# Kernel optimization log

Measured on AMD Instinct MI355X. Metric: run time of the kernel, lower is better.

The kernel has to match this reference:

```python
import jax, jax.numpy as jnp
import numpy as np

C1, C2, NUM_HEADS = 128, 128, 8
N, H_A, W_A = 2, 200, 200
H_B, W_B = 100, 360


def _polar_coords(fov, gh, gw, H, W):
    # Pixel-space polar sampling grid, matching torch linspace semantics.
    cx, cy = W // 2, H // 2
    t = jnp.arange(gw, dtype=jnp.float32) / (gw - 1)
    angles = -fov / 2 + fov * t                      # [gw]
    ca, sa = jnp.cos(angles), jnp.sin(angles)
    rmax = jnp.minimum(cx / jnp.abs(ca), cy / jnp.abs(sa))
    r = (jnp.arange(gh, dtype=jnp.float32) / (gh - 1))[:, None] * rmax[None, :]  # [gh,gw]
    x = jnp.clip(cx + r * ca, 0.0, W - 1.0)
    y = jnp.clip(cy - r * sa, 0.0, H - 1.0)
    return x, y


def _bilinear(bev, x, y):
    # grid_sample(mode='bilinear', align_corners=True) with in-range clamped coords.
    C, H, W = bev.shape
    x0 = jnp.floor(x); y0 = jnp.floor(y)
    wx = x - x0; wy = y - y0
    x0i = jnp.clip(x0.astype(jnp.int32), 0, W - 1)
    x1i = jnp.clip(x0i + 1, 0, W - 1)
    y0i = jnp.clip(y0.astype(jnp.int32), 0, H - 1)
    y1i = jnp.clip(y0i + 1, 0, H - 1)
    v00 = bev[:, y0i, x0i]; v01 = bev[:, y0i, x1i]
    v10 = bev[:, y1i, x0i]; v11 = bev[:, y1i, x1i]
    return v00 * (1 - wx) * (1 - wy) + v01 * wx * (1 - wy) + v10 * (1 - wx) * wy + v11 * wx * wy


def _restore(rect, fov, H, W):
    # scatter-add restore with count normalization (rrestore_bev_map).
    C, gh, gw = rect.shape
    x, y = _polar_coords(fov, gh, gw, H, W)
    xi = jnp.clip(jnp.round(x).astype(jnp.int32), 0, W - 1)
    yi = jnp.clip(jnp.round(y).astype(jnp.int32), 0, H - 1)
    idx = (yi * W + xi).reshape(-1)
    vals = rect.reshape(C, -1)
    acc = jnp.zeros((C, H * W), rect.dtype).at[:, idx].add(vals)
    cnt = jnp.zeros((H * W,), rect.dtype).at[idx].add(jnp.ones_like(idx, rect.dtype))
    cnt = jnp.where(cnt == 0, jnp.ones_like(cnt), cnt)
    return (acc / cnt).reshape(C, H, W)


def _mha(q, k, v, in_w, in_b, out_w, out_b, nheads):
    # torch.nn.MultiheadAttention (batch_first, eval mode -> dropout inactive).
    B, Lq, E = q.shape
    Lk = k.shape[1]
    hd = E // nheads
    wq, wk, wv = jnp.split(in_w, 3)
    bq, bk, bv = jnp.split(in_b, 3)
    qh = (q @ wq.T + bq).reshape(B, Lq, nheads, hd).transpose(0, 2, 1, 3)
    kh = (k @ wk.T + bk).reshape(B, Lk, nheads, hd).transpose(0, 2, 1, 3)
    vh = (v @ wv.T + bv).reshape(B, Lk, nheads, hd).transpose(0, 2, 1, 3)
    scores = jnp.einsum('bhqd,bhkd->bhqk', qh, kh) / jnp.sqrt(jnp.asarray(hd, q.dtype))
    attn = jax.nn.softmax(scores, axis=-1)
    o = jnp.einsum('bhqk,bhkd->bhqd', attn, vh).transpose(0, 2, 1, 3).reshape(B, Lq, E)
    return o @ out_w.T + out_b


def setup_inputs() -> dict:
    key = jax.random.key(0)
    ks = jax.random.split(key, 12)
    s1 = 1.0 / np.sqrt(C1)
    s2 = 1.0 / np.sqrt(C2)
    return {
        'list_a': jax.random.normal(ks[0], (N, C1, H_A, W_A), jnp.float32),
        'list_b': jax.random.normal(ks[1], (N, C2, H_B, W_B), jnp.float32),
        'fov_list': jax.random.uniform(ks[2], (N,), jnp.float32, 0.5 * np.pi, 0.9 * np.pi),
        'rots_list': jax.random.normal(ks[3], (N, 3, 3), jnp.float32),
        'trans_list': jax.random.normal(ks[4], (N, 3), jnp.float32),
        'Wq': jax.random.normal(ks[5], (C1, C1), jnp.float32) * s1,
        'bq': jnp.zeros((C1,), jnp.float32),
        'Wk': jax.random.normal(ks[6], (C1, C2), jnp.float32) * s2,
        'bk': jnp.zeros((C1,), jnp.float32),
        'Wv': jax.random.normal(ks[7], (C1, C2), jnp.float32) * s2,
        'bv': jnp.zeros((C1,), jnp.float32),
        'in_proj_w': jax.random.normal(ks[8], (3 * C1, C1), jnp.float32) * s1,
        'in_proj_b': jnp.zeros((3 * C1,), jnp.float32),
        'out_w': jax.random.normal(ks[9], (C1, C1), jnp.float32) * s1,
        'out_b': jnp.zeros((C1,), jnp.float32),
    }


def reference(list_a, list_b, fov_list, rots_list, trans_list,
              Wq, bq, Wk, bk, Wv, bv, in_proj_w, in_proj_b, out_w, out_b):
    def per_sample(a, b, fov):
        c1, h1, w1 = a.shape
        c2, h2, w2 = b.shape
        # extract rectangular (polar resample) of a onto (h1, w2) grid
        x, y = _polar_coords(fov, h1, w2, h1, w1)
        a_rect = _bilinear(a, x, y)                 # [C1, h1, w2]
        a_seq = a_rect.transpose(2, 1, 0)           # [w2, h1, C1]
        b_seq = b.transpose(2, 1, 0)                # [w2, h2, C2]
        q = a_seq @ Wq.T + bq
        k = b_seq @ Wk.T + bk
        v = b_seq @ Wv.T + bv
        o = _mha(q, k, v, in_proj_w, in_proj_b, out_w, out_b, NUM_HEADS)
        a_enh = o.transpose(2, 1, 0)                # [C1, h1, w2]
        return a + _restore(a_enh, fov, h1, w1)
    return jax.vmap(per_sample)(list_a, list_b, fov_list)
```

## Files before the change

kernel.cpp:

```cpp
#include <hip/hip_runtime.h>
#include <hip/hip_bf16.h>
#include <math.h>

#define C1N 128
#define HA 200
#define WA 200
#define HBB 100
#define WBB 360
#define GH 200
#define GW 360
#define NHD 8
#define HDD 16

typedef __attribute__((ext_vector_type(8))) short short8;
typedef __attribute__((ext_vector_type(4))) float f32x4;
typedef __attribute__((ext_vector_type(16))) float f32x16;

__device__ __forceinline__ float bf2f(unsigned short u) {
  union { unsigned int i; float f; } c; c.i = ((unsigned int)u) << 16; return c.f;
}
__device__ __forceinline__ unsigned short f2bf(float f) {
  __hip_bfloat16 h = __float2bfloat16(f);
  unsigned short u;
  __builtin_memcpy(&u, &h, sizeof(u));
  return u;
}

__device__ __forceinline__ void polar_xy(float fov, int i, int j, float& x, float& y) {
#pragma clang fp contract(off)
  float t = (float)j / 359.0f;
  float angle = -fov / 2.0f + fov * t;
  float ca = (float)cos((double)angle);
  float sa = (float)sin((double)angle);
  float rmax = fminf(100.0f / fabsf(ca), 100.0f / fabsf(sa));
  float r = ((float)i / 199.0f) * rmax;
  float xv = 100.0f + r * ca;
  float yv = 100.0f - r * sa;
  x = fminf(fmaxf(xv, 0.0f), 199.0f);
  y = fminf(fmaxf(yv, 0.0f), 199.0f);
}

__global__ void weff_k(const float* __restrict__ Wq, const float* __restrict__ Wk,
                       const float* __restrict__ Wv, const float* __restrict__ bq,
                       const float* __restrict__ bk, const float* __restrict__ bv,
                       const float* __restrict__ inw, const float* __restrict__ inb,
                       const float* __restrict__ outw, const float* __restrict__ outb,
                       __hip_bfloat16* __restrict__ Wb, float* __restrict__ beff) {
  int which = blockIdx.y;
  int o = blockIdx.x;
  int kcol = threadIdx.x;
  if (which == 3) {
    Wb[3 * 16384 + o * 128 + kcol] = __float2bfloat16(outw[o * 128 + kcol]);
    if (kcol == 0) beff[384 + o] = outb[o];
    return;
  }
  const float* Wx = (which == 0) ? Wq : ((which == 1) ? Wk : Wv);
  const float* bx = (which == 0) ? bq : ((which == 1) ? bk : bv);
  const float* wrow = inw + (which * 128 + o) * 128;
  float acc = 0.0f;
  for (int m = 0; m < 128; ++m) acc += wrow[m] * Wx[m * 128 + kcol];
  Wb[which * 16384 + o * 128 + kcol] = __float2bfloat16(acc);
  if (kcol == 0) {
    float bacc = inb[which * 128 + o];
    for (int m = 0; m < 128; ++m) bacc += wrow[m] * bx[m];
    beff[which * 128 + o] = bacc;
  }
}

__global__ __launch_bounds__(256) void transA_k(const float* __restrict__ a,
                                                __hip_bfloat16* __restrict__ aT) {
  __shared__ float tile[32][33];
  int p0 = blockIdx.x * 32, c0 = blockIdx.y * 32;
  int tp = threadIdx.x & 31, tr = threadIdx.x >> 5;
  for (int cc = tr; cc < 32; cc += 8)
    tile[cc][tp] = a[(size_t)(c0 + cc) * 40000 + p0 + tp];
  __syncthreads();
  for (int pp = tr; pp < 32; pp += 8)
    aT[(size_t)(p0 + pp) * C1N + c0 + tp] = __float2bfloat16(tile[tp][pp]);
}

__global__ __launch_bounds__(256) void bilinear2_k(const __hip_bfloat16* __restrict__ aT,
                                                   const float* __restrict__ fovp, int n,
                                                   __hip_bfloat16* __restrict__ aseq) {
  __shared__ float sw[20][4];
  __shared__ int sp[20][4];
  int j = blockIdx.x;
  int i_base = blockIdx.y * 20;
  int t = threadIdx.x;
  if (t < 20) {
    float x, y;
    polar_xy(fovp[n], i_base + t, j, x, y);
    float x0f = floorf(x), y0f = floorf(y);
    float wx = x - x0f, wy = y - y0f;
    int x0 = max(0, min(199, (int)x0f));
    int x1 = min(x0 + 1, 199);
    int y0 = max(0, min(199, (int)y0f));
    int y1 = min(y0 + 1, 199);
    sp[t][0] = y0 * 200 + x0; sp[t][1] = y0 * 200 + x1;
    sp[t][2] = y1 * 200 + x0; sp[t][3] = y1 * 200 + x1;
    sw[t][0] = (1.0f - wx) * (1.0f - wy); sw[t][1] = wx * (1.0f - wy);
    sw[t][2] = (1.0f - wx) * wy;          sw[t][3] = wx * wy;
  }
  __syncthreads();
  int lane = t & 63, wv = t >> 6;
  for (int ii = wv; ii < 20; ii += 4) {
    int i = i_base + ii;
    float w00 = sw[ii][0], w01 = sw[ii][1], w10 = sw[ii][2], w11 = sw[ii][3];
    ushort2 u00 = ((const ushort2*)(aT + (size_t)sp[ii][0] * C1N))[lane];
    ushort2 u01 = ((const ushort2*)(aT + (size_t)sp[ii][1] * C1N))[lane];
    ushort2 u10 = ((const ushort2*)(aT + (size_t)sp[ii][2] * C1N))[lane];
    ushort2 u11 = ((const ushort2*)(aT + (size_t)sp[ii][3] * C1N))[lane];
    float v0 = w00 * bf2f(u00.x) + w01 * bf2f(u01.x) + w10 * bf2f(u10.x) + w11 * bf2f(u11.x);
    float v1 = w00 * bf2f(u00.y) + w01 * bf2f(u01.y) + w10 * bf2f(u10.y) + w11 * bf2f(u11.y);
    ushort2 outv; outv.x = f2bf(v0); outv.y = f2bf(v1);
    ((ushort2*)(aseq + (size_t)(j * GH + i) * C1N))[lane] = outv;
  }
}

__global__ __launch_bounds__(256) void transpose_k(const float* __restrict__ b,
                                                   __hip_bfloat16* __restrict__ bs) {
  __shared__ float tile[32][33];
  int kk = blockIdx.z;
  int j0 = blockIdx.x * 32, c0 = blockIdx.y * 32;
  int tj = threadIdx.x & 31;
  int tr = threadIdx.x >> 5;
  for (int cc = tr; cc < 32; cc += 8) {
    int gj = j0 + tj;
    tile[cc][tj] = (gj < WBB) ? b[(c0 + cc) * (HBB * WBB) + kk * WBB + gj] : 0.0f;
  }
  __syncthreads();
  for (int jj = tr; jj < 32; jj += 8) {
    int gj = j0 + jj;
    if (gj < WBB)
      bs[(size_t)(gj * HBB + kk) * C1N + c0 + (threadIdx.x & 31)] =
          __float2bfloat16(tile[threadIdx.x & 31][jj]);
  }
}

__device__ __forceinline__ void gemm16_mfma(const unsigned short* __restrict__ A,
                                            const unsigned short* __restrict__ W,
                                            int m_base, f32x4 acc[8]) {
  int lane = threadIdx.x & 63;
  int col = lane & 15, quad = lane >> 4;
#pragma unroll
  for (int nt = 0; nt < 8; ++nt) acc[nt] = (f32x4)0.0f;
#pragma unroll
  for (int s = 0; s < 4; ++s) {
    short8 aF = *(const short8*)&A[(size_t)(m_base + col) * 128 + s * 32 + quad * 8];
#pragma unroll
    for (int nt = 0; nt < 8; ++nt) {
      short8 bF = *(const short8*)&W[(size_t)(nt * 16 + col) * 128 + s * 32 + quad * 8];
      acc[nt] = __builtin_amdgcn_mfma_f32_16x16x32_bf16(aF, bF, acc[nt], 0, 0, 0);
    }
  }
}

__device__ __forceinline__ void stage_bf16(unsigned short (*tile)[136],
                                           const f32x4 acc[8],
                                           const float* __restrict__ bias) {
  int lane = threadIdx.x & 63, wv = threadIdx.x >> 6;
  int col = lane & 15, quad = lane >> 4;
#pragma unroll
  for (int nt = 0; nt < 8; ++nt) {
    float bb = bias[nt * 16 + col];
#pragma unroll
    for (int r = 0; r < 4; ++r)
      tile[wv * 16 + quad * 4 + r][nt * 16 + col] = f2bf(acc[nt][r] + bb);
  }
  __syncthreads();
}

__global__ __launch_bounds__(256) void gemm_q_k(const unsigned short* __restrict__ A,
                                                const unsigned short* __restrict__ Wb,
                                                const float* __restrict__ beff,
                                                unsigned short* __restrict__ qb) {
  __shared__ unsigned short tile[64][136];
  int m0 = blockIdx.x * 64;
  f32x4 acc[8];
  gemm16_mfma(A, Wb, m0 + (threadIdx.x >> 6) * 16, acc);
  stage_bf16(tile, acc, beff);
  for (int u = threadIdx.x; u < 1024; u += 256) {
    int rl = u >> 4, ch = (u & 15) * 8;
    *(short8*)&qb[(size_t)(m0 + rl) * 128 + ch] = *(const short8*)&tile[rl][ch];
  }
}

__global__ __launch_bounds__(256) void gemm_kv_k(const unsigned short* __restrict__ A,
                                                 const unsigned short* __restrict__ Wb,
                                                 const float* __restrict__ beff,
                                                 unsigned short* __restrict__ kb,
                                                 unsigned short* __restrict__ vT) {
  __shared__ unsigned short tile[64][136];
  int which = blockIdx.y;
  int m0 = blockIdx.x * 64;
  f32x4 acc[8];
  gemm16_mfma(A, Wb + (which ? 32768 : 16384), m0 + (threadIdx.x >> 6) * 16, acc);
  stage_bf16(tile, acc, beff + (which ? 256 : 128));
  if (which == 0) {
    for (int u = threadIdx.x; u < 1024; u += 256) {
      int rl = u >> 4, ch = (u & 15) * 8;
      int row = m0 + rl;
      if (row < 36000) {
        int jj = row / 100, key = row - jj * 100;
        *(short8*)&kb[((size_t)jj * 128 + key) * 128 + ch] = *(const short8*)&tile[rl][ch];
      }
    }
  } else {
    for (int u = threadIdx.x; u < 8192; u += 256) {
      int cc = u >> 6, kl = u & 63;
      int row = m0 + kl;
      if (row < 36000) {
        int jj = row / 100, key = row - jj * 100;
        vT[((size_t)jj * 128 + cc) * 128 + key] = tile[kl][cc];
      }
    }
  }
}

__global__ __launch_bounds__(512) void attn6_k(const unsigned short* __restrict__ qb,
                                               const unsigned short* __restrict__ kb,
                                               const unsigned short* __restrict__ vT,
                                               unsigned short* __restrict__ o) {
  __shared__ unsigned short Ps[8][32][120];
  __shared__ unsigned short Osh[32][136];
  int d = blockIdx.x;
  int xcd = d & 7, idx = d >> 3;
  int j = xcd * 45 + idx % 45;
  int mt = idx / 45;
  int h = threadIdx.x >> 6;
  int lane = threadIdx.x & 63;
  int col = lane & 31, half = lane >> 5;

  short8 qF = *(const short8*)&qb[(size_t)(j * 200 + mt * 32 + col) * 128 + h * 16 + half * 8];
  f32x16 S[4];
#pragma unroll
  for (int nt = 0; nt < 4; ++nt) {
    short8 kF = *(const short8*)&kb[((size_t)j * 128 + nt * 32 + col) * 128 + h * 16 + half * 8];
    S[nt] = __builtin_amdgcn_mfma_f32_32x32x16_bf16(kF, qF, (f32x16)0.0f, 0, 0, 0);
  }

  float rsum = 0.0f;
#pragma unroll
  for (int nt = 0; nt < 3; ++nt)
#pragma unroll
    for (int r = 0; r < 16; ++r) {
      float e = __expf(S[nt][r] * 0.25f);
      S[nt][r] = e; rsum += e;
    }
#pragma unroll
  for (int r = 0; r < 16; ++r) {
    float e = (half == 0 && r < 4) ? __expf(S[3][r] * 0.25f) : 0.0f;
    S[3][r] = e; rsum += e;
  }
  rsum += __shfl_xor(rsum, 32, 64);
  float inv = __fdividef(1.0f, rsum);

#pragma unroll
  for (int nt = 0; nt < 4; ++nt) {
#pragma unroll
    for (int g = 0; g < 4; ++g) {
      if (nt == 3 && g >= 2) continue;
      float e0 = S[nt][4 * g + 0] * inv, e1 = S[nt][4 * g + 1] * inv;
      float e2 = S[nt][4 * g + 2] * inv, e3 = S[nt][4 * g + 3] * inv;
      unsigned int lo, hi;
      asm("v_cvt_pk_bf16_f32 %0, %1, %2" : "=v"(lo) : "v"(e0), "v"(e1));
      asm("v_cvt_pk_bf16_f32 %0, %1, %2" : "=v"(hi) : "v"(e2), "v"(e3));
      *(uint2*)&Ps[h][col][nt * 32 + 8 * g + 4 * half] = make_uint2(lo, hi);
    }
  }

  short8 ones;
#pragma unroll
  for (int i = 0; i < 8; ++i) ones[i] = (short)0x3F80;
  const unsigned short* vrow = &vT[((size_t)j * 128 + h * 16 + (col & 15)) * 128];
  f32x16 O = (f32x16)0.0f;
#pragma unroll
  for (int ks = 0; ks < 7; ++ks) {
    short8 aP = *(const short8*)&Ps[h][col][ks * 16 + half * 8];
    short8 bV = (col < 16) ? *(const short8*)&vrow[ks * 16 + half * 8] : ones;
    O = __builtin_amdgcn_mfma_f32_32x32x16_bf16(aP, bV, O, 0, 0, 0);
  }
#pragma unroll
  for (int r = 0; r < 16; ++r) {
    int row = (r & 3) + 8 * (r >> 2) + 4 * half;
    if (col < 16) Osh[row][h * 16 + col] = f2bf(O[r]);
  }
  __syncthreads();
  int rl = threadIdx.x >> 4, ch = (threadIdx.x & 15) * 8;
  int qr = mt * 32 + rl;
  if (qr < 200)
    *(short8*)&o[(size_t)(j * 200 + qr) * 128 + ch] = *(const short8*)&Osh[rl][ch];
}

__global__ __launch_bounds__(256) void gemm_os_k(const unsigned short* __restrict__ A,
                                                 const unsigned short* __restrict__ Wb,
                                                 const float* __restrict__ beff,
                                                 const float* __restrict__ fovp, int n,
                                                 float* __restrict__ accP,
                                                 float* __restrict__ cnt) {
  __shared__ float tile[64][132];
  __shared__ int sidx[64];
  int m0 = blockIdx.x * 64;
  int t = threadIdx.x;
  f32x4 acc[8];
  gemm16_mfma(A, Wb + 49152, m0 + (t >> 6) * 16, acc);
  if (t < 64) {
    int m = m0 + t;
    int j = m / 200, i = m - j * 200;
    float x, y;
    polar_xy(fovp[n], i, j, x, y);
    int xi = (int)rintf(x); xi = max(0, min(199, xi));
    int yi = (int)rintf(y); yi = max(0, min(199, yi));
    sidx[t] = yi * 200 + xi;
    atomicAdd(&cnt[yi * 200 + xi], 1.0f);
  }
  {
    int lane = t & 63, wv = t >> 6;
    int col = lane & 15, quad = lane >> 4;
#pragma unroll
    for (int nt = 0; nt < 8; ++nt) {
      float bb = beff[384 + nt * 16 + col];
#pragma unroll
      for (int r = 0; r < 4; ++r)
        tile[wv * 16 + quad * 4 + r][nt * 16 + col] = acc[nt][r] + bb;
    }
  }
  __syncthreads();
  int c = t & 127, half = t >> 7;
  int r0 = half * 32;
  int cur = sidx[r0];
  float sum = 0.0f;
#pragma unroll 4
  for (int r = r0; r < r0 + 32; ++r) {
    float v = tile[r][c];
    int idx = sidx[r];
    if (idx != cur) {
      atomicAdd(&accP[(size_t)cur * C1N + c], sum);
      cur = idx;
      sum = v;
    } else {
      sum += v;
    }
  }
  atomicAdd(&accP[(size_t)cur * C1N + c], sum);
}

__global__ __launch_bounds__(256) void finalize2_k(const float* __restrict__ a,
                                                   const float* __restrict__ accP,
                                                   const float* __restrict__ cnt,
                                                   float* __restrict__ out) {
  __shared__ float tile[64][129];
  __shared__ float sinv[64];
  int p0 = blockIdx.x * 64;
  int t = threadIdx.x;
  if (t < 64) {
    float cv = cnt[p0 + t];
    sinv[t] = 1.0f / (cv == 0.0f ? 1.0f : cv);
  }
  for (int u = t; u < 64 * 128; u += 256) {
    int pp = u >> 7, c = u & 127;
    tile[pp][c] = accP[(size_t)(p0 + pp) * C1N + c];
  }
  __syncthreads();
  for (int u = t; u < 64 * 128; u += 256) {
    int pp = u & 63, c = u >> 6;
    int g = c * 40000 + p0 + pp;
    out[g] = a[g] + tile[pp][c] * sinv[pp];
  }
}

extern "C" void kernel_launch(void* const* d_in, const int* in_sizes, int n_in,
                              void* d_out, int out_size, void* d_ws, size_t ws_size,
                              hipStream_t stream) {
  const float* list_a = (const float*)d_in[0];
  const float* list_b = (const float*)d_in[1];
  const float* fov   = (const float*)d_in[2];
  const float* Wq    = (const float*)d_in[5];
  const float* bq    = (const float*)d_in[6];
  const float* Wk    = (const float*)d_in[7];
  const float* bk    = (const float*)d_in[8];
  const float* Wv    = (const float*)d_in[9];
  const float* bv    = (const float*)d_in[10];
  const float* inw   = (const float*)d_in[11];
  const float* inb   = (const float*)d_in[12];
  const float* outw  = (const float*)d_in[13];
  const float* outb  = (const float*)d_in[14];
  float* out = (float*)d_out;
  float* ws = (float*)d_ws;

  float* beff = ws;
  __hip_bfloat16* Wb = (__hip_bfloat16*)(ws + 512);
  float* P2 = ws + 512 + 32768;
  float* qb_f = P2 + 9216000;
  float* kb_f = qb_f + 4620288;
  float* vT_f = kb_f + 2949120;
  float* P0_f = vT_f + 2949120;
  float* P1_f = P0_f + 4620288;
  float* cnt  = P1_f + 2310144;

  unsigned short* qb = (unsigned short*)qb_f;
  unsigned short* kb = (unsigned short*)kb_f;
  unsigned short* vT = (unsigned short*)vT_f;
  __hip_bfloat16* P0 = (__hip_bfloat16*)P0_f;
  __hip_bfloat16* P1 = (__hip_bfloat16*)P1_f;
  __hip_bfloat16* aT = (__hip_bfloat16*)P2;
  float* accP = P2;

  weff_k<<<dim3(128, 4), 128, 0, stream>>>(Wq, Wk, Wv, bq, bk, bv, inw, inb, outw, outb, Wb, beff);

  for (int n = 0; n < 2; ++n) {
    const float* a_n = list_a + (size_t)n * C1N * HA * WA;
    const float* b_n = list_b + (size_t)n * C1N * HBB * WBB;
    float* out_n = out + (size_t)n * C1N * HA * WA;

    (void)hipMemsetAsync(cnt, 0, (size_t)HA * WA * sizeof(float), stream);

    transA_k<<<dim3(1250, 4), 256, 0, stream>>>(a_n, aT);
    bilinear2_k<<<dim3(GW, 10), 256, 0, stream>>>(aT, fov, n, P0);
    (void)hipMemsetAsync(accP, 0, (size_t)HA * WA * C1N * sizeof(float), stream);
    transpose_k<<<dim3(12, 4, 100), 256, 0, stream>>>(b_n, P1);
    gemm_kv_k<<<dim3(563, 2), 256, 0, stream>>>((const unsigned short*)P1,
                                                (const unsigned short*)Wb, beff, kb, vT);
    gemm_q_k<<<1125, 256, 0, stream>>>((const unsigned short*)P0,
                                       (const unsigned short*)Wb, beff, qb);
    attn6_k<<<2520, 512, 0, stream>>>(qb, kb, vT, (unsigned short*)P0);
    gemm_os_k<<<1125, 256, 0, stream>>>((const unsigned short*)P0,
                                        (const unsigned short*)Wb, beff, fov, n,
                                        accP, cnt);
    finalize2_k<<<625, 256, 0, stream>>>(a_n, accP, cnt, out_n);
  }
}
```

Before: 507.5 us.

## Replace atomic scatter-add restore with counting-sort gather

```diff
diff --git a/kernel.cpp b/kernel.cpp
--- a/kernel.cpp
+++ b/kernel.cpp
@@ -217,6 +217,32 @@
   }
 }
 
+__global__ __launch_bounds__(256) void gemm_o_k(const unsigned short* __restrict__ A,
+                                                const unsigned short* __restrict__ Wb,
+                                                const float* __restrict__ beff,
+                                                float* __restrict__ C) {
+  __shared__ float tile[64][132];
+  int m0 = blockIdx.x * 64;
+  f32x4 acc[8];
+  gemm16_mfma(A, Wb + 49152, m0 + (threadIdx.x >> 6) * 16, acc);
+  {
+    int lane = threadIdx.x & 63, wv = threadIdx.x >> 6;
+    int col = lane & 15, quad = lane >> 4;
+#pragma unroll
+    for (int nt = 0; nt < 8; ++nt) {
+      float bb = beff[384 + nt * 16 + col];
+#pragma unroll
+      for (int r = 0; r < 4; ++r)
+        tile[wv * 16 + quad * 4 + r][nt * 16 + col] = acc[nt][r] + bb;
+    }
+  }
+  __syncthreads();
+  for (int u = threadIdx.x; u < 2048; u += 256) {
+    int rl = u >> 5, ch = (u & 31) * 4;
+    *(f32x4*)&C[(size_t)(m0 + rl) * 128 + ch] = *(const f32x4*)&tile[rl][ch];
+  }
+}
+
 __global__ __launch_bounds__(512) void attn6_k(const unsigned short* __restrict__ qb,
                                                const unsigned short* __restrict__ kb,
                                                const unsigned short* __restrict__ vT,
@@ -292,71 +318,100 @@
     *(short8*)&o[(size_t)(j * 200 + qr) * 128 + ch] = *(const short8*)&Osh[rl][ch];
 }
 
-__global__ __launch_bounds__(256) void gemm_os_k(const unsigned short* __restrict__ A,
-                                                 const unsigned short* __restrict__ Wb,
-                                                 const float* __restrict__ beff,
-                                                 const float* __restrict__ fovp, int n,
-                                                 float* __restrict__ accP,
-                                                 float* __restrict__ cnt) {
-  __shared__ float tile[64][132];
-  __shared__ int sidx[64];
-  int m0 = blockIdx.x * 64;
-  int t = threadIdx.x;
-  f32x4 acc[8];
-  gemm16_mfma(A, Wb + 49152, m0 + (t >> 6) * 16, acc);
-  if (t < 64) {
-    int m = m0 + t;
-    int j = m / 200, i = m - j * 200;
-    float x, y;
-    polar_xy(fovp[n], i, j, x, y);
-    int xi = (int)rintf(x); xi = max(0, min(199, xi));
-    int yi = (int)rintf(y); yi = max(0, min(199, yi));
-    sidx[t] = yi * 200 + xi;
-    atomicAdd(&cnt[yi * 200 + xi], 1.0f);
-  }
-  {
-    int lane = t & 63, wv = t >> 6;
-    int col = lane & 15, quad = lane >> 4;
-#pragma unroll
-    for (int nt = 0; nt < 8; ++nt) {
-      float bb = beff[384 + nt * 16 + col];
-#pragma unroll
-      for (int r = 0; r < 4; ++r)
-        tile[wv * 16 + quad * 4 + r][nt * 16 + col] = acc[nt][r] + bb;
-    }
-  }
-  __syncthreads();
-  int c = t & 127, half = t >> 7;
-  int r0 = half * 32;
-  int cur = sidx[r0];
-  float sum = 0.0f;
-#pragma unroll 4
-  for (int r = r0; r < r0 + 32; ++r) {
-    float v = tile[r][c];
-    int idx = sidx[r];
-    if (idx != cur) {
-      atomicAdd(&accP[(size_t)cur * C1N + c], sum);
-      cur = idx;
-      sum = v;
-    } else {
-      sum += v;
-    }
-  }
-  atomicAdd(&accP[(size_t)cur * C1N + c], sum);
-}
-
-__global__ __launch_bounds__(256) void finalize2_k(const float* __restrict__ a,
+__global__ __launch_bounds__(256) void count_k(const float* __restrict__ fovp, int n,
+                                               int* __restrict__ pid,
+                                               int* __restrict__ counts) {
+  int m = blockIdx.x * 256 + threadIdx.x;
+  if (m >= 72000) return;
+  int j = m / 200, i = m - j * 200;
+  float x, y;
+  polar_xy(fovp[n], i, j, x, y);
+  int xi = (int)rintf(x); xi = max(0, min(199, xi));
+  int yi = (int)rintf(y); yi = max(0, min(199, yi));
+  int p = yi * 200 + xi;
+  pid[m] = p;
+  atomicAdd(counts + p, 1);
+}
+
+__global__ __launch_bounds__(256) void sumv_k(const int* __restrict__ counts,
+                                              int* __restrict__ bsum) {
+  __shared__ int sred[4];
+  int b = blockIdx.x, t = threadIdx.x;
+  int s = 0;
+  for (int u = t; u < 1000; u += 256) s += counts[b * 1000 + u];
+  for (int off = 32; off; off >>= 1) s += __shfl_down(s, off, 64);
+  if ((t & 63) == 0) sred[t >> 6] = s;
+  __syncthreads();
+  if (t == 0) bsum[b] = sred[0] + sred[1] + sred[2] + sred[3];
+}
+
+__global__ __launch_bounds__(64) void scanf_k(const int* __restrict__ counts,
+                                              const int* __restrict__ bsum,
+                                              int* __restrict__ offs,
+                                              int* __restrict__ cursor) {
+  __shared__ int sc[1000];
+  int b = blockIdx.x, t = threadIdx.x;
+  for (int u = t; u < 1000; u += 64) sc[u] = counts[b * 1000 + u];
+  __syncthreads();
+  if (t == 0) {
+    int run = 0;
+    for (int q = 0; q < b; ++q) run += bsum[q];
+    for (int u = 0; u < 1000; ++u) { int v = sc[u]; sc[u] = run; run += v; }
+  }
+  __syncthreads();
+  for (int u = t; u < 1000; u += 64) {
+    int o = sc[u];
+    offs[b * 1000 + u] = o;
+    cursor[b * 1000 + u] = o;
+  }
+}
+
+__global__ __launch_bounds__(256) void fill_k(const int* __restrict__ pid,
+                                              int* __restrict__ cursor,
+                                              int* __restrict__ srcm) {
+  int m = blockIdx.x * 256 + threadIdx.x;
+  if (m >= 72000) return;
+  int slot = atomicAdd(cursor + pid[m], 1);
+  srcm[slot] = m;
+}
+
+__global__ __launch_bounds__(256) void gather_k(const float* __restrict__ aenh,
+                                                const int* __restrict__ offs,
+                                                const int* __restrict__ counts,
+                                                const int* __restrict__ srcm,
+                                                float* __restrict__ accP) {
+  int W = blockIdx.x * 4 + (threadIdx.x >> 6);
+  int lane = threadIdx.x & 63;
+  for (int k = 0; k < 16; ++k) {
+    int p = W + 2500 * k;
+    int nsz = counts[p], s0 = offs[p];
+    float sx = 0.0f, sy = 0.0f;
+    for (int q0 = 0; q0 < nsz; q0 += 16) {
+      const float* rp[16];
+#pragma unroll
+      for (int u = 0; u < 16; ++u) {
+        int q = min(q0 + u, nsz - 1);
+        int m = srcm[s0 + q];
+        rp[u] = aenh + (size_t)m * 128 + 2 * lane;
+      }
+#pragma unroll
+      for (int u = 0; u < 16; ++u) {
+        float2 r = *(const float2*)rp[u];
+        if (q0 + u < nsz) { sx += r.x; sy += r.y; }
+      }
+    }
+    float inv = (nsz > 0) ? 1.0f / (float)nsz : 0.0f;
+    float2 o2; o2.x = sx * inv; o2.y = sy * inv;
+    *(float2*)&accP[(size_t)p * C1N + 2 * lane] = o2;
+  }
+}
+
+__global__ __launch_bounds__(256) void finalize3_k(const float* __restrict__ a,
                                                    const float* __restrict__ accP,
-                                                   const float* __restrict__ cnt,
                                                    float* __restrict__ out) {
   __shared__ float tile[64][129];
-  __shared__ float sinv[64];
   int p0 = blockIdx.x * 64;
   int t = threadIdx.x;
-  if (t < 64) {
-    float cv = cnt[p0 + t];
-    sinv[t] = 1.0f / (cv == 0.0f ? 1.0f : cv);
-  }
   for (int u = t; u < 64 * 128; u += 256) {
     int pp = u >> 7, c = u & 127;
     tile[pp][c] = accP[(size_t)(p0 + pp) * C1N + c];
@@ -365,7 +420,7 @@
   for (int u = t; u < 64 * 128; u += 256) {
     int pp = u & 63, c = u >> 6;
     int g = c * 40000 + p0 + pp;
-    out[g] = a[g] + tile[pp][c] * sinv[pp];
+    out[g] = a[g] + tile[pp][c];
   }
 }
 
@@ -396,7 +451,6 @@
   float* vT_f = kb_f + 2949120;
   float* P0_f = vT_f + 2949120;
   float* P1_f = P0_f + 4620288;
-  float* cnt  = P1_f + 2310144;
 
   unsigned short* qb = (unsigned short*)qb_f;
   unsigned short* kb = (unsigned short*)kb_f;
@@ -404,7 +458,15 @@
   __hip_bfloat16* P0 = (__hip_bfloat16*)P0_f;
   __hip_bfloat16* P1 = (__hip_bfloat16*)P1_f;
   __hip_bfloat16* aT = (__hip_bfloat16*)P2;
-  float* accP = P2;
+  float* aenh = P2;
+  float* accP = qb_f;
+
+  int* pid    = (int*)P1_f;
+  int* counts = pid + 72000;
+  int* offs   = counts + 40000;
+  int* cursor = offs + 40000;
+  int* srcm   = cursor + 40000;
+  int* bsum   = srcm + 72000;
 
   weff_k<<<dim3(128, 4), 128, 0, stream>>>(Wq, Wk, Wv, bq, bk, bv, inw, inb, outw, outb, Wb, beff);
 
@@ -413,20 +475,23 @@
     const float* b_n = list_b + (size_t)n * C1N * HBB * WBB;
     float* out_n = out + (size_t)n * C1N * HA * WA;
 
-    (void)hipMemsetAsync(cnt, 0, (size_t)HA * WA * sizeof(float), stream);
-
     transA_k<<<dim3(1250, 4), 256, 0, stream>>>(a_n, aT);
     bilinear2_k<<<dim3(GW, 10), 256, 0, stream>>>(aT, fov, n, P0);
-    (void)hipMemsetAsync(accP, 0, (size_t)HA * WA * C1N * sizeof(float), stream);
     transpose_k<<<dim3(12, 4, 100), 256, 0, stream>>>(b_n, P1);
     gemm_kv_k<<<dim3(563, 2), 256, 0, stream>>>((const unsigned short*)P1,
                                                 (const unsigned short*)Wb, beff, kb, vT);
+    (void)hipMemsetAsync(counts, 0, 40000 * sizeof(int), stream);
+    count_k<<<282, 256, 0, stream>>>(fov, n, pid, counts);
+    sumv_k<<<40, 256, 0, stream>>>(counts, bsum);
+    scanf_k<<<40, 64, 0, stream>>>(counts, bsum, offs, cursor);
+    fill_k<<<282, 256, 0, stream>>>(pid, cursor, srcm);
+
     gemm_q_k<<<1125, 256, 0, stream>>>((const unsigned short*)P0,
                                        (const unsigned short*)Wb, beff, qb);
     attn6_k<<<2520, 512, 0, stream>>>(qb, kb, vT, (unsigned short*)P0);
-    gemm_os_k<<<1125, 256, 0, stream>>>((const unsigned short*)P0,
-                                        (const unsigned short*)Wb, beff, fov, n,
-                                        accP, cnt);
-    finalize2_k<<<625, 256, 0, stream>>>(a_n, accP, cnt, out_n);
-  }
-}
+    gemm_o_k<<<1125, 256, 0, stream>>>((const unsigned short*)P0,
+                                       (const unsigned short*)Wb, beff, aenh);
+    gather_k<<<625, 256, 0, stream>>>(aenh, offs, counts, srcm, accP);
+    finalize3_k<<<625, 256, 0, stream>>>(a_n, accP, out_n);
+  }
+}
```

After: 728.1 us. 43.5% more time.

## Fuse Q projection GEMM into attention kernel and write output in place

Applied to the files above, without the earlier changes.

```diff
diff --git a/kernel.cpp b/kernel.cpp
--- a/kernel.cpp
+++ b/kernel.cpp
@@ -170,21 +170,6 @@
   __syncthreads();
 }
 
-__global__ __launch_bounds__(256) void gemm_q_k(const unsigned short* __restrict__ A,
-                                                const unsigned short* __restrict__ Wb,
-                                                const float* __restrict__ beff,
-                                                unsigned short* __restrict__ qb) {
-  __shared__ unsigned short tile[64][136];
-  int m0 = blockIdx.x * 64;
-  f32x4 acc[8];
-  gemm16_mfma(A, Wb, m0 + (threadIdx.x >> 6) * 16, acc);
-  stage_bf16(tile, acc, beff);
-  for (int u = threadIdx.x; u < 1024; u += 256) {
-    int rl = u >> 4, ch = (u & 15) * 8;
-    *(short8*)&qb[(size_t)(m0 + rl) * 128 + ch] = *(const short8*)&tile[rl][ch];
-  }
-}
-
 __global__ __launch_bounds__(256) void gemm_kv_k(const unsigned short* __restrict__ A,
                                                  const unsigned short* __restrict__ Wb,
                                                  const float* __restrict__ beff,
@@ -217,12 +202,13 @@
   }
 }
 
-__global__ __launch_bounds__(512) void attn6_k(const unsigned short* __restrict__ qb,
+__global__ __launch_bounds__(512) void attn7_k(unsigned short* __restrict__ aseq_o,
                                                const unsigned short* __restrict__ kb,
                                                const unsigned short* __restrict__ vT,
-                                               unsigned short* __restrict__ o) {
+                                               const unsigned short* __restrict__ Wb,
+                                               const float* __restrict__ beff) {
   __shared__ unsigned short Ps[8][32][120];
-  __shared__ unsigned short Osh[32][136];
+  __shared__ unsigned short qos[32][136];
   int d = blockIdx.x;
   int xcd = d & 7, idx = d >> 3;
   int j = xcd * 45 + idx % 45;
@@ -230,8 +216,36 @@
   int h = threadIdx.x >> 6;
   int lane = threadIdx.x & 63;
   int col = lane & 31, half = lane >> 5;
-
-  short8 qF = *(const short8*)&qb[(size_t)(j * 200 + mt * 32 + col) * 128 + h * 16 + half * 8];
+  int col16 = lane & 15, quad = lane >> 4;
+
+  {
+    int rs = h & 1;
+    int ng = h >> 1;
+    int m_base = j * 200 + mt * 32 + rs * 16;
+    f32x4 qacc[2];
+    qacc[0] = (f32x4)0.0f; qacc[1] = (f32x4)0.0f;
+#pragma unroll
+    for (int s = 0; s < 4; ++s) {
+      short8 aF = *(const short8*)&aseq_o[(size_t)(m_base + col16) * 128 + s * 32 + quad * 8];
+#pragma unroll
+      for (int i = 0; i < 2; ++i) {
+        int nt = ng * 2 + i;
+        short8 bF = *(const short8*)&Wb[(size_t)(nt * 16 + col16) * 128 + s * 32 + quad * 8];
+        qacc[i] = __builtin_amdgcn_mfma_f32_16x16x32_bf16(aF, bF, qacc[i], 0, 0, 0);
+      }
+    }
+#pragma unroll
+    for (int i = 0; i < 2; ++i) {
+      int nt = ng * 2 + i;
+      float bb = beff[nt * 16 + col16];
+#pragma unroll
+      for (int r = 0; r < 4; ++r)
+        qos[rs * 16 + quad * 4 + r][nt * 16 + col16] = f2bf(qacc[i][r] + bb);
+    }
+  }
+  __syncthreads();
+
+  short8 qF = *(const short8*)&qos[col][h * 16 + half * 8];
   f32x16 S[4];
 #pragma unroll
   for (int nt = 0; nt < 4; ++nt) {
@@ -272,7 +286,7 @@
   short8 ones;
 #pragma unroll
   for (int i = 0; i < 8; ++i) ones[i] = (short)0x3F80;
-  const unsigned short* vrow = &vT[((size_t)j * 128 + h * 16 + (col & 15)) * 128];
+  const unsigned short* vrow = &vT[((size_t)j * 128 + h * 16 + col16) * 128];
   f32x16 O = (f32x16)0.0f;
 #pragma unroll
   for (int ks = 0; ks < 7; ++ks) {
@@ -280,16 +294,17 @@
     short8 bV = (col < 16) ? *(const short8*)&vrow[ks * 16 + half * 8] : ones;
     O = __builtin_amdgcn_mfma_f32_32x32x16_bf16(aP, bV, O, 0, 0, 0);
   }
+  __syncthreads();
 #pragma unroll
   for (int r = 0; r < 16; ++r) {
     int row = (r & 3) + 8 * (r >> 2) + 4 * half;
-    if (col < 16) Osh[row][h * 16 + col] = f2bf(O[r]);
+    if (col < 16) qos[row][h * 16 + col] = f2bf(O[r]);
   }
   __syncthreads();
   int rl = threadIdx.x >> 4, ch = (threadIdx.x & 15) * 8;
   int qr = mt * 32 + rl;
   if (qr < 200)
-    *(short8*)&o[(size_t)(j * 200 + qr) * 128 + ch] = *(const short8*)&Osh[rl][ch];
+    *(short8*)&aseq_o[(size_t)(j * 200 + qr) * 128 + ch] = *(const short8*)&qos[rl][ch];
 }
 
 __global__ __launch_bounds__(256) void gemm_os_k(const unsigned short* __restrict__ A,
@@ -398,7 +413,6 @@
   float* P1_f = P0_f + 4620288;
   float* cnt  = P1_f + 2310144;
 
-  unsigned short* qb = (unsigned short*)qb_f;
   unsigned short* kb = (unsigned short*)kb_f;
   unsigned short* vT = (unsigned short*)vT_f;
   __hip_bfloat16* P0 = (__hip_bfloat16*)P0_f;
@@ -421,9 +435,8 @@
     transpose_k<<<dim3(12, 4, 100), 256, 0, stream>>>(b_n, P1);
     gemm_kv_k<<<dim3(563, 2), 256, 0, stream>>>((const unsigned short*)P1,
                                                 (const unsigned short*)Wb, beff, kb, vT);
-    gemm_q_k<<<1125, 256, 0, stream>>>((const unsigned short*)P0,
-                                       (const unsigned short*)Wb, beff, qb);
-    attn6_k<<<2520, 512, 0, stream>>>(qb, kb, vT, (unsigned short*)P0);
+    attn7_k<<<2520, 512, 0, stream>>>((unsigned short*)P0, kb, vT,
+                                      (const unsigned short*)Wb, beff);
     gemm_os_k<<<1125, 256, 0, stream>>>((const unsigned short*)P0,
                                         (const unsigned short*)Wb, beff, fov, n,
                                         accP, cnt);
```

Measured after the change: 506.1 us. Within noise of the previous version (-0.3%).
